# Performance work log

Hardware: AMD Instinct MI355X
Metric: run time of the kernel (lower is better)

## Reference

```python
import jax, jax.numpy as jnp
import numpy as np

B, H, W, KS = 2, 352, 1216, 3  # KITTI depth completion, 3x3 deformable kernel


def setup_inputs() -> dict:
    key = jax.random.key(0)
    k1, k2, k3 = jax.random.split(key, 3)
    K = KS * KS
    depth = jax.random.uniform(k1, (B, 1, H, W), dtype=jnp.float32)
    weight = jax.random.uniform(k2, (B, K, H, W), dtype=jnp.float32)
    offset = jax.random.normal(k3, (B, 2 * K, H, W), dtype=jnp.float32)
    w = jnp.ones((1, 1, KS, KS), dtype=jnp.float32)  # nn.Parameter(torch.ones)
    b = jnp.zeros((1,), dtype=jnp.float32)           # nn.Parameter(torch.zeros)
    return {"depth": depth, "weight": weight, "offset": offset, "w": w, "b": b}


def _dcn_v2_post(depth, weight, offset, w, b):
    # depth: [B,1,H,W], weight(mask): [B,K,H,W], offset: [B,2K,H,W]
    Bn, _, Hn, Wn = depth.shape
    k = w.shape[-1]
    pad = (k - 1) // 2
    K = k * k
    # dkn_residual=True -> zero-mean normalize modulation over kernel channel
    weight = weight - jnp.mean(weight, axis=1, keepdims=True)
    # DCNv2 offset layout: per kernel tap idx=i*k+j, channels (2*idx, 2*idx+1) = (dy, dx)
    off = offset.reshape(Bn, K, 2, Hn, Wn)
    ky = jnp.arange(k, dtype=depth.dtype) - pad  # stride=1, dilation=1
    kyy = jnp.repeat(ky, k).reshape(1, K, 1, 1)  # row offset per tap
    kxx = jnp.tile(ky, k).reshape(1, K, 1, 1)    # col offset per tap
    py = jnp.arange(Hn, dtype=depth.dtype).reshape(1, 1, Hn, 1) + kyy + off[:, :, 0]
    px = jnp.arange(Wn, dtype=depth.dtype).reshape(1, 1, 1, Wn) + kxx + off[:, :, 1]
    y0 = jnp.floor(py)
    x0 = jnp.floor(px)
    fy = py - y0  # bilinear fractions
    fx = px - x0
    y0i = y0.astype(jnp.int32)
    x0i = x0.astype(jnp.int32)
    d_flat = depth.reshape(Bn, Hn * Wn)

    def gather(yi, xi):
        # zero-padded gather: out-of-bounds corners contribute 0 (matches DCNv2 CUDA)
        valid = (yi >= 0) & (yi < Hn) & (xi >= 0) & (xi < Wn)
        idx = jnp.clip(yi, 0, Hn - 1) * Wn + jnp.clip(xi, 0, Wn - 1)
        v = jnp.take_along_axis(d_flat, idx.reshape(Bn, -1), axis=1).reshape(idx.shape)
        return jnp.where(valid, v, jnp.zeros((), depth.dtype))

    v00 = gather(y0i, x0i)
    v01 = gather(y0i, x0i + 1)
    v10 = gather(y0i + 1, x0i)
    v11 = gather(y0i + 1, x0i + 1)
    val = (v00 * (1 - fy) * (1 - fx) + v01 * (1 - fy) * fx
           + v10 * fy * (1 - fx) + v11 * fy * fx)  # [B,K,H,W]
    # 1-in/1-out channel conv: weighted sum over K taps of (mask * sampled value)
    out = jnp.einsum('k,bkhw->bhw', w.reshape(K), weight * val)[:, None] + b[0]
    return out + depth  # dkn_residual add


def reference(depth, weight, offset, w, b):
    return _dcn_v2_post(depth, weight, offset, w, b)
```

## Files before the change

### kernel.cpp

```cpp
#include <hip/hip_runtime.h>

#define B_ 2
#define H_ 352
#define W_ 1216
#define HW_ (H_ * W_)
#define K_ 9
#define TW 64
#define TH 8
#define SOFF 8
#define SR (TH + 2 * SOFF)
#define SC (TW + 2 * SOFF)
#define NBX (W_ / TW)
#define NBY (H_ / TH)
#define NBLK (B_ * NBX * NBY)
#define NV4 (SR * (SC / 4))

typedef float v4 __attribute__((ext_vector_type(4)));

__global__ __launch_bounds__(512) void dcn_post_kernel(
    const float* __restrict__ depth,
    const float* __restrict__ weight,
    const float* __restrict__ offset,
    const float* __restrict__ wtap,
    const float* __restrict__ bias,
    float* __restrict__ out)
{
    __shared__ float sm[SR * SC];

    const int bid = blockIdx.x;
    const int b   = bid / (NBX * NBY);
    const int r2  = bid - b * (NBX * NBY);
    const int by  = r2 / NBX;
    const int bx  = r2 - by * NBX;
    const int tid = threadIdx.x;
    const int tx  = tid & (TW - 1);
    const int ty  = tid >> 6;

    const int y  = by * TH + ty;
    const int x  = bx * TW + tx;
    const int oy = by * TH - SOFF;
    const int ox = bx * TW - SOFF;
    const int p  = y * W_ + x;

    const float* __restrict__ dpt = depth + b * HW_;

    if (tid < NV4) {
        const int r  = tid / (SC / 4);
        const int c4 = (tid - r * (SC / 4)) * 4;
        const int gy = oy + r;
        const int gx = ox + c4;
        v4 v = 0.f;
        if ((unsigned)gy < (unsigned)H_ && (unsigned)gx < (unsigned)W_)
            v = *reinterpret_cast<const v4*>(dpt + gy * W_ + gx);
        *reinterpret_cast<v4*>(sm + r * SC + c4) = v;
    }

    const float bv = bias[0];

    const float* obase = offset + (size_t)b * 2 * K_ * HW_ + p;
    float ody[K_], odx[K_];
#pragma unroll
    for (int k = 0; k < K_; ++k) {
        ody[k] = obase[(2 * k) * HW_];
        odx[k] = obase[(2 * k + 1) * HW_];
    }

    const float* wbase = weight + (size_t)b * K_ * HW_ + p;
    float cf[K_];
    float m = 0.f;
#pragma unroll
    for (int k = 0; k < K_; ++k) {
        cf[k] = wbase[k * HW_];
        m += cf[k];
    }
    m *= (1.f / 9.f);
#pragma unroll
    for (int k = 0; k < K_; ++k)
        cf[k] = (cf[k] - m) * wtap[k];

    __syncthreads();

    const float dval = sm[(ty + SOFF) * SC + (tx + SOFF)];

    float acc = 0.f;
#pragma unroll
    for (int k = 0; k < K_; ++k) {
        const float py = (float)(y + (k / 3) - 1) + ody[k];
        const float px = (float)(x + (k % 3) - 1) + odx[k];
        const float y0f = floorf(py);
        const float x0f = floorf(px);
        const float fy = py - y0f;
        const float fx = px - x0f;
        const int yi0 = (int)y0f, xi0 = (int)x0f;

        const int ly = yi0 - oy;
        const int lx = xi0 - ox;
        float v00, v01, v10, v11;
        if ((unsigned)ly <= (SR - 2) && (unsigned)lx <= (SC - 2)) {
            const float* s = sm + ly * SC + lx;
            v00 = s[0];
            v01 = s[1];
            v10 = s[SC];
            v11 = s[SC + 1];
        } else {
            const int yi1 = yi0 + 1, xi1 = xi0 + 1;
            const bool vy0 = (unsigned)yi0 < (unsigned)H_;
            const bool vy1 = (unsigned)yi1 < (unsigned)H_;
            const bool vx0 = (unsigned)xi0 < (unsigned)W_;
            const bool vx1 = (unsigned)xi1 < (unsigned)W_;
            const int r0 = yi0 * W_;
            const int r1 = r0 + W_;
            v00 = (vy0 && vx0) ? dpt[r0 + xi0] : 0.f;
            v01 = (vy0 && vx1) ? dpt[r0 + xi1] : 0.f;
            v10 = (vy1 && vx0) ? dpt[r1 + xi0] : 0.f;
            v11 = (vy1 && vx1) ? dpt[r1 + xi1] : 0.f;
        }

        const float a  = fmaf(fx, v01 - v00, v00);
        const float c  = fmaf(fx, v11 - v10, v10);
        const float val = fmaf(fy, c - a, a);
        acc = fmaf(cf[k], val, acc);
    }

    out[b * HW_ + p] = acc + bv + dval;
}

extern "C" void kernel_launch(void* const* d_in, const int* in_sizes, int n_in,
                              void* d_out, int out_size, void* d_ws, size_t ws_size,
                              hipStream_t stream) {
    const float* depth  = (const float*)d_in[0];
    const float* weight = (const float*)d_in[1];
    const float* offset = (const float*)d_in[2];
    const float* wtap   = (const float*)d_in[3];
    const float* bias   = (const float*)d_in[4];
    float* out = (float*)d_out;

    dim3 grid(NBLK), block(512);
    hipLaunchKernelGGL(dcn_post_kernel, grid, block, 0, stream,
                       depth, weight, offset, wtap, bias, out);
}
```

Baseline: 25.23 us.

## Process two rows per thread with taller tile and prefetched second-row loads

Doubles the tile height so each thread computes two output pixels, eight rows apart. The shared depth halo is amortized over twice as many outputs, which cuts redundant halo loads. The second pixel's offset and weight loads are issued before the first pixel's taps are computed, overlapping memory latency with compute. This costs more registers, which may lower occupancy, and halves the number of blocks.

```diff
diff --git a/kernel.cpp b/kernel.cpp
--- a/kernel.cpp
+++ b/kernel.cpp
@@ -6,7 +6,7 @@
 #define HW_ (H_ * W_)
 #define K_ 9
 #define TW 64
-#define TH 8
+#define TH 16
 #define SOFF 8
 #define SR (TH + 2 * SOFF)
 #define SC (TW + 2 * SOFF)
@@ -17,71 +17,11 @@
 
 typedef float v4 __attribute__((ext_vector_type(4)));
 
-__global__ __launch_bounds__(512) void dcn_post_kernel(
-    const float* __restrict__ depth,
-    const float* __restrict__ weight,
-    const float* __restrict__ offset,
-    const float* __restrict__ wtap,
-    const float* __restrict__ bias,
-    float* __restrict__ out)
+__device__ __forceinline__ float dcn_taps(
+    const float* __restrict__ sm, const float* __restrict__ dpt,
+    int oy, int ox, int y, int x,
+    const float* ody, const float* odx, const float* cf)
 {
-    __shared__ float sm[SR * SC];
-
-    const int bid = blockIdx.x;
-    const int b   = bid / (NBX * NBY);
-    const int r2  = bid - b * (NBX * NBY);
-    const int by  = r2 / NBX;
-    const int bx  = r2 - by * NBX;
-    const int tid = threadIdx.x;
-    const int tx  = tid & (TW - 1);
-    const int ty  = tid >> 6;
-
-    const int y  = by * TH + ty;
-    const int x  = bx * TW + tx;
-    const int oy = by * TH - SOFF;
-    const int ox = bx * TW - SOFF;
-    const int p  = y * W_ + x;
-
-    const float* __restrict__ dpt = depth + b * HW_;
-
-    if (tid < NV4) {
-        const int r  = tid / (SC / 4);
-        const int c4 = (tid - r * (SC / 4)) * 4;
-        const int gy = oy + r;
-        const int gx = ox + c4;
-        v4 v = 0.f;
-        if ((unsigned)gy < (unsigned)H_ && (unsigned)gx < (unsigned)W_)
-            v = *reinterpret_cast<const v4*>(dpt + gy * W_ + gx);
-        *reinterpret_cast<v4*>(sm + r * SC + c4) = v;
-    }
-
-    const float bv = bias[0];
-
-    const float* obase = offset + (size_t)b * 2 * K_ * HW_ + p;
-    float ody[K_], odx[K_];
-#pragma unroll
-    for (int k = 0; k < K_; ++k) {
-        ody[k] = obase[(2 * k) * HW_];
-        odx[k] = obase[(2 * k + 1) * HW_];
-    }
-
-    const float* wbase = weight + (size_t)b * K_ * HW_ + p;
-    float cf[K_];
-    float m = 0.f;
-#pragma unroll
-    for (int k = 0; k < K_; ++k) {
-        cf[k] = wbase[k * HW_];
-        m += cf[k];
-    }
-    m *= (1.f / 9.f);
-#pragma unroll
-    for (int k = 0; k < K_; ++k)
-        cf[k] = (cf[k] - m) * wtap[k];
-
-    __syncthreads();
-
-    const float dval = sm[(ty + SOFF) * SC + (tx + SOFF)];
-
     float acc = 0.f;
 #pragma unroll
     for (int k = 0; k < K_; ++k) {
@@ -96,7 +36,7 @@
         const int ly = yi0 - oy;
         const int lx = xi0 - ox;
         float v00, v01, v10, v11;
-        if ((unsigned)ly <= (SR - 2) && (unsigned)lx <= (SC - 2)) {
+        if (__builtin_expect((unsigned)ly <= (SR - 2) && (unsigned)lx <= (SC - 2), 1)) {
             const float* s = sm + ly * SC + lx;
             v00 = s[0];
             v01 = s[1];
@@ -121,8 +61,118 @@
         const float val = fmaf(fy, c - a, a);
         acc = fmaf(cf[k], val, acc);
     }
+    return acc;
+}
 
-    out[b * HW_ + p] = acc + bv + dval;
+__global__ __launch_bounds__(512) void dcn_post_kernel(
+    const float* __restrict__ depth,
+    const float* __restrict__ weight,
+    const float* __restrict__ offset,
+    const float* __restrict__ wtap,
+    const float* __restrict__ bias,
+    float* __restrict__ out)
+{
+    __shared__ float sm[SR * SC];
+
+    const int bid = blockIdx.x;
+    const int b   = bid / (NBX * NBY);
+    const int r2  = bid - b * (NBX * NBY);
+    const int by  = r2 / NBX;
+    const int bx  = r2 - by * NBX;
+    const int tid = threadIdx.x;
+    const int tx  = tid & (TW - 1);
+    const int ty  = tid >> 6;
+
+    const int y0 = by * TH;
+    const int x  = bx * TW + tx;
+    const int yA = y0 + ty;
+    const int yB = yA + 8;
+    const int oy = y0 - SOFF;
+    const int ox = bx * TW - SOFF;
+    const int pA = yA * W_ + x;
+    const int pB = pA + 8 * W_;
+
+    const float* __restrict__ dpt = depth + b * HW_;
+
+    {
+        const int i = tid;
+        const int r  = i / (SC / 4);
+        const int c4 = (i - r * (SC / 4)) * 4;
+        const int gy = oy + r;
+        const int gx = ox + c4;
+        v4 v = 0.f;
+        if ((unsigned)gy < (unsigned)H_ && (unsigned)gx < (unsigned)W_)
+            v = *reinterpret_cast<const v4*>(dpt + gy * W_ + gx);
+        *reinterpret_cast<v4*>(sm + r * SC + c4) = v;
+    }
+    if (tid < NV4 - 512) {
+        const int i = tid + 512;
+        const int r  = i / (SC / 4);
+        const int c4 = (i - r * (SC / 4)) * 4;
+        const int gy = oy + r;
+        const int gx = ox + c4;
+        v4 v = 0.f;
+        if ((unsigned)gy < (unsigned)H_ && (unsigned)gx < (unsigned)W_)
+            v = *reinterpret_cast<const v4*>(dpt + gy * W_ + gx);
+        *reinterpret_cast<v4*>(sm + r * SC + c4) = v;
+    }
+
+    const float bv = bias[0];
+    float wt[K_];
+#pragma unroll
+    for (int k = 0; k < K_; ++k) wt[k] = wtap[k];
+
+    const float* obaseA = offset + (size_t)b * 2 * K_ * HW_ + pA;
+    float odyA[K_], odxA[K_];
+#pragma unroll
+    for (int k = 0; k < K_; ++k) {
+        odyA[k] = obaseA[(2 * k) * HW_];
+        odxA[k] = obaseA[(2 * k + 1) * HW_];
+    }
+    const float* wbaseA = weight + (size_t)b * K_ * HW_ + pA;
+    float cfA[K_];
+    float mA = 0.f;
+#pragma unroll
+    for (int k = 0; k < K_; ++k) {
+        cfA[k] = wbaseA[k * HW_];
+        mA += cfA[k];
+    }
+    mA *= (1.f / 9.f);
+#pragma unroll
+    for (int k = 0; k < K_; ++k) cfA[k] = (cfA[k] - mA) * wt[k];
+
+    __syncthreads();
+
+    const float* obaseB = offset + (size_t)b * 2 * K_ * HW_ + pB;
+    float odyB[K_], odxB[K_], wgB[K_];
+#pragma unroll
+    for (int k = 0; k < K_; ++k) {
+        odyB[k] = obaseB[(2 * k) * HW_];
+        odxB[k] = obaseB[(2 * k + 1) * HW_];
+    }
+    const float* wbaseB = weight + (size_t)b * K_ * HW_ + pB;
+#pragma unroll
+    for (int k = 0; k < K_; ++k) wgB[k] = wbaseB[k * HW_];
+
+    {
+        const float dvalA = sm[(ty + SOFF) * SC + (tx + SOFF)];
+        const float accA = dcn_taps(sm, dpt, oy, ox, yA, x, odyA, odxA, cfA);
+        out[b * HW_ + pA] = accA + bv + dvalA;
+    }
+
+    {
+        float cfB[K_];
+        float mB = 0.f;
+#pragma unroll
+        for (int k = 0; k < K_; ++k) mB += wgB[k];
+        mB *= (1.f / 9.f);
+#pragma unroll
+        for (int k = 0; k < K_; ++k) cfB[k] = (wgB[k] - mB) * wt[k];
+
+        const float dvalB = sm[(ty + 8 + SOFF) * SC + (tx + SOFF)];
+        const float accB = dcn_taps(sm, dpt, oy, ox, yB, x, odyB, odxB, cfB);
+        out[b * HW_ + pB] = accB + bv + dvalB;
+    }
 }
 
 extern "C" void kernel_launch(void* const* d_in, const int* in_sizes, int n_in,
```

New measurement: 25.36 us. About the same (+0.5%).
